# Kernel tuning notes

Hardware: AMD Instinct MI355X
Metric: run time of the kernel (lower is better)

Reference implementation:

```python
import jax, jax.numpy as jnp
import numpy as np

B, S, H, NH, FF = 8, 512, 1024, 16, 4096
DK = H // NH


def _ln(x, g, b):
    m = x.mean(-1, keepdims=True)
    v = ((x - m) ** 2).mean(-1, keepdims=True)
    return (x - m) / jnp.sqrt(v + 1e-5) * g + b


def _fwd(x, predicate_pos, attn_bias, attention_mask, atom_graph, variable_graph,
         ln1_g, ln1_b, wq, bq, wk, bk, wv, bv, wo, bo,
         pq_w, pq_b, pk_w, pk_b, pv_w, pv_b, ln2_g, ln2_b, w1, b1, w2, b2):
    b_, s_, h_ = x.shape
    y = _ln(x, ln1_g, ln1_b)
    # ---- self attention (manual MHA with additive bias + mask) ----
    scale = DK ** -0.5
    q = (y @ wq + bq).reshape(b_, s_, NH, DK) * scale
    k = (y @ wk + bk).reshape(b_, s_, NH, DK)
    v = (y @ wv + bv).reshape(b_, s_, NH, DK)
    scores = jnp.einsum('bihd,bjhd->bhij', q, k)
    scores = scores + attn_bias[:, None, :, :] + attention_mask[:, None, :, :]
    att = jax.nn.softmax(scores, axis=-1)
    y_self = jnp.einsum('bhij,bjhd->bihd', att, v).reshape(b_, s_, h_) @ wo + bo
    # ---- path attention (single-head with graph biases) ----
    pscale = h_ ** -0.5
    pq = (y @ pq_w + pq_b) * pscale
    pk = y @ pk_w + pk_b
    pv = y @ pv_w + pv_b
    patt = jnp.einsum('bid,bjd->bij', pq, pk) + atom_graph + variable_graph
    patt = jax.nn.softmax(patt, axis=-1)
    xp = jnp.einsum('bij,bjd->bid', patt, pv)  # [B,S,H]
    # vectorized gather-mean over predicate positions (replaces per-sample loop)
    prev = jnp.concatenate([xp[:, :1], xp[:, :-1]], axis=1)   # xp[i-1]
    nxt = jnp.concatenate([xp[:, 1:], xp[:, -1:]], axis=1)    # xp[i+1]
    a0 = xp[:, 0:2].mean(axis=1, keepdims=True)               # i == 0
    a1 = xp[:, 0:3].mean(axis=1, keepdims=True)               # i == 1
    a2 = (xp + nxt) / 2.0                                     # pos[i-2] == 1
    a3 = (prev + xp + nxt) / 3.0                              # else
    i_arr = jnp.arange(s_)
    pos = (predicate_pos == 1)
    pos_m2 = jnp.pad(pos[:, :-2], ((0, 0), (2, 0)))           # pos[i-2], False for i<2
    atom = jnp.where(pos_m2[..., None], a2, a3)
    atom = jnp.where((i_arr == 1)[None, :, None], a1, atom)
    atom = jnp.where((i_arr == 0)[None, :, None], a0, atom)
    w = pos.astype(xp.dtype)
    path = (atom * w[..., None]).sum(1) / w.sum(1, keepdims=True)  # [B,H]
    y_path = jnp.broadcast_to(path[:, None, :], (b_, s_, h_))
    # ---- combine + residual + FFN ----
    x = x + (y_self + y_path) / 2.0
    y2 = _ln(x, ln2_g, ln2_b)
    hmid = jax.nn.gelu(y2 @ w1 + b1, approximate=False)
    return x + (hmid @ w2 + b2)


def setup_inputs() -> dict:
    key = jax.random.key(0)
    ks = jax.random.split(key, 16)
    def w(k, shape):
        return 0.02 * jax.random.normal(k, shape, dtype=jnp.float32)
    pp = jax.random.randint(ks[0], (B, S), 0, 2, dtype=jnp.int32)
    pp = pp.at[:, 2].set(1).at[:, -1].set(0)  # >=1 predicate; no predicate at last node
    return {
        'x': jax.random.normal(ks[1], (B, S, H), dtype=jnp.float32),
        'predicate_pos': pp,
        'variable_tags': jnp.zeros((B, S), dtype=jnp.int32),
        'attn_bias': 0.1 * jax.random.normal(ks[2], (B, S, S), dtype=jnp.float32),
        'attention_mask': jnp.zeros((B, S, S), dtype=jnp.float32),
        'atom_graph': 0.1 * jax.random.normal(ks[3], (B, S, S), dtype=jnp.float32),
        'variable_graph': 0.1 * jax.random.normal(ks[4], (B, S, S), dtype=jnp.float32),
        'ln1_g': jnp.ones((H,), jnp.float32), 'ln1_b': jnp.zeros((H,), jnp.float32),
        'wq': w(ks[5], (H, H)), 'bq': jnp.zeros((H,), jnp.float32),
        'wk': w(ks[6], (H, H)), 'bk': jnp.zeros((H,), jnp.float32),
        'wv': w(ks[7], (H, H)), 'bv': jnp.zeros((H,), jnp.float32),
        'wo': w(ks[8], (H, H)), 'bo': jnp.zeros((H,), jnp.float32),
        'pq_w': w(ks[9], (H, H)), 'pq_b': jnp.zeros((H,), jnp.float32),
        'pk_w': w(ks[10], (H, H)), 'pk_b': jnp.zeros((H,), jnp.float32),
        'pv_w': w(ks[11], (H, H)), 'pv_b': jnp.zeros((H,), jnp.float32),
        'ln2_g': jnp.ones((H,), jnp.float32), 'ln2_b': jnp.zeros((H,), jnp.float32),
        'w1': w(ks[12], (H, FF)), 'b1': jnp.zeros((FF,), jnp.float32),
        'w2': w(ks[13], (FF, H)), 'b2': jnp.zeros((H,), jnp.float32),
    }


def reference(x, predicate_pos, variable_tags, attn_bias, attention_mask, atom_graph, variable_graph,
              ln1_g, ln1_b, wq, bq, wk, bk, wv, bv, wo, bo,
              pq_w, pq_b, pk_w, pk_b, pv_w, pv_b, ln2_g, ln2_b, w1, b1, w2, b2):
    # variable_tags is unused in the original forward as well
    return _fwd(x, predicate_pos, attn_bias, attention_mask, atom_graph, variable_graph,
                ln1_g, ln1_b, wq, bq, wk, bk, wv, bv, wo, bo,
                pq_w, pq_b, pk_w, pk_b, pv_w, pv_b, ln2_g, ln2_b, w1, b1, w2, b2)
```

## Files before the change

### kernel.cpp

```cpp
#include <hip/hip_runtime.h>
#include <hip/hip_bf16.h>
#include <math.h>


typedef __bf16 bf16x8 __attribute__((ext_vector_type(8)));
typedef float f32x4 __attribute__((ext_vector_type(4)));

__device__ __forceinline__ void async_copy16(void* lds, const void* g) {
  __builtin_amdgcn_global_load_lds(
      (__attribute__((address_space(1))) void*)(void*)g,
      (__attribute__((address_space(3))) void*)lds, 16, 0, 0);
}

__global__ __launch_bounds__(256) void ln_rows_bf16(
    const float* __restrict__ X, const float* __restrict__ G,
    const float* __restrict__ Bt, __hip_bfloat16* __restrict__ O) {
  long row = blockIdx.x;
  int t = threadIdx.x;
  const float4 xv = ((const float4*)(X + row * 1024))[t];
  float s = xv.x + xv.y + xv.z + xv.w;
  float q = xv.x * xv.x + xv.y * xv.y + xv.z * xv.z + xv.w * xv.w;
#pragma unroll
  for (int o = 32; o; o >>= 1) {
    s += __shfl_xor(s, o);
    q += __shfl_xor(q, o);
  }
  __shared__ float rs[4], rq[4];
  int wid = t >> 6;
  if ((t & 63) == 0) { rs[wid] = s; rq[wid] = q; }
  __syncthreads();
  s = rs[0] + rs[1] + rs[2] + rs[3];
  q = rq[0] + rq[1] + rq[2] + rq[3];
  float mean = s * (1.f / 1024.f);
  float var = q * (1.f / 1024.f) - mean * mean;
  float rstd = rsqrtf(var + 1e-5f);
  const float4 gv = ((const float4*)G)[t];
  const float4 bv = ((const float4*)Bt)[t];
  __hip_bfloat16* o = O + row * 1024 + t * 4;
  o[0] = __float2bfloat16((xv.x - mean) * rstd * gv.x + bv.x);
  o[1] = __float2bfloat16((xv.y - mean) * rstd * gv.y + bv.y);
  o[2] = __float2bfloat16((xv.z - mean) * rstd * gv.z + bv.z);
  o[3] = __float2bfloat16((xv.w - mean) * rstd * gv.w + bv.w);
}

struct TC7 {
  const float* in[7];
  __hip_bfloat16* out[7];
  float scale[7];
};
__global__ __launch_bounds__(256) void tconv7(TC7 p) {
  __shared__ float t[32][33];
  int j = blockIdx.z;
  const float* in = p.in[j];
  __hip_bfloat16* out = p.out[j];
  float sc = p.scale[j];
  int c0 = blockIdx.x * 32, r0 = blockIdx.y * 32;
  int tid = threadIdx.x;
  int lr = tid >> 3, lc = (tid & 7) * 4;
  const float4 v = *(const float4*)&in[(long)(r0 + lr) * 1024 + c0 + lc];
  t[lr][lc] = v.x; t[lr][lc + 1] = v.y; t[lr][lc + 2] = v.z; t[lr][lc + 3] = v.w;
  __syncthreads();
  int oc = tid >> 3, orr = (tid & 7) * 4;
  __hip_bfloat16* o = &out[(long)(c0 + oc) * 1024 + r0 + orr];
  o[0] = __float2bfloat16(t[orr][oc] * sc);
  o[1] = __float2bfloat16(t[orr + 1][oc] * sc);
  o[2] = __float2bfloat16(t[orr + 2][oc] * sc);
  o[3] = __float2bfloat16(t[orr + 3][oc] * sc);
}

__global__ __launch_bounds__(256) void tconv_f32_bf16(
    const float* __restrict__ in, __hip_bfloat16* __restrict__ out, int R,
    int C) {
  __shared__ float t[32][33];
  int c0 = blockIdx.x * 32, r0 = blockIdx.y * 32;
  int tid = threadIdx.x;
  int lr = tid >> 3, lc = (tid & 7) * 4;
  const float4 v = *(const float4*)&in[(long)(r0 + lr) * C + c0 + lc];
  t[lr][lc] = v.x; t[lr][lc + 1] = v.y; t[lr][lc + 2] = v.z; t[lr][lc + 3] = v.w;
  __syncthreads();
  int oc = tid >> 3, orr = (tid & 7) * 4;
  __hip_bfloat16* o = &out[(long)(c0 + oc) * R + r0 + orr];
  o[0] = __float2bfloat16(t[orr][oc]);
  o[1] = __float2bfloat16(t[orr + 1][oc]);
  o[2] = __float2bfloat16(t[orr + 2][oc]);
  o[3] = __float2bfloat16(t[orr + 3][oc]);
}

__global__ __launch_bounds__(256) void tconv_bf16(
    const __hip_bfloat16* __restrict__ in, __hip_bfloat16* __restrict__ out,
    int R, int C, int ldin, long sIn) {
  __shared__ __hip_bfloat16 t[32][34];
  int bz = blockIdx.z;
  long ibase = (long)bz * sIn;
  long obase = (long)bz * R * C;
  int c0 = blockIdx.x * 32, r0 = blockIdx.y * 32;
  int tid = threadIdx.x;
  int lr = tid >> 3, lc = (tid & 7) * 4;
  const __hip_bfloat16* ip = &in[ibase + (long)(r0 + lr) * ldin + c0 + lc];
  t[lr][lc] = ip[0]; t[lr][lc + 1] = ip[1]; t[lr][lc + 2] = ip[2]; t[lr][lc + 3] = ip[3];
  __syncthreads();
  int oc = tid >> 3, orr = (tid & 7) * 4;
  __hip_bfloat16* o = &out[obase + (long)(c0 + oc) * R + r0 + orr];
  o[0] = t[orr][oc];
  o[1] = t[orr + 1][oc];
  o[2] = t[orr + 2][oc];
  o[3] = t[orr + 3][oc];
}

struct BC6 {
  const float* b[6];
  float scale[6];
};
__global__ __launch_bounds__(256) void bias_concat(BC6 p, float* __restrict__ o) {
  int idx = blockIdx.x * 256 + threadIdx.x;
  int j = idx >> 10, e = idx & 1023;
  o[idx] = p.b[j][e] * p.scale[j];
}

template <int BN>
__global__ __launch_bounds__(512, 2) void gemm256(
    const __hip_bfloat16* __restrict__ A, const __hip_bfloat16* __restrict__ Bt,
    const float* __restrict__ bias, void* __restrict__ C, int K, int lda,
    int ldb, int ldc, int act, int obf, long sC) {
  constexpr int NR = BN / 64;
  constexpr int ABYTES = 256 * 128;
  constexpr int BBYTES = BN * 128;
  constexpr int BUF = ABYTES + BBYTES;
  __shared__ char lds[2 * BUF];

  int nwg = gridDim.x * gridDim.y;
  int wg = blockIdx.y * gridDim.x + blockIdx.x;
  int cpx = nwg >> 3;
  int sw = (wg & 7) * cpx + (wg >> 3);
  int bx = sw % gridDim.x, by = sw / gridDim.x;
  const int m0 = by * 256, n0 = bx * BN;
  const int z = blockIdx.z;
  const long kbase = (long)z * K * 2;

  const int tid = threadIdx.x;
  const int lane = tid & 63, wid = tid >> 6;
  const int wm = wid >> 2, wn = wid & 3;
  const int ll = lane & 15, lh = lane >> 4;

  const char* Ag = (const char*)A;
  const char* Bg = (const char*)Bt;
  const int srow = tid >> 3;
  const int scb = (tid & 7) * 16;

  auto stage = [&](int t, int bsel) {
    char* base = lds + bsel * BUF;
    long kb = kbase + (long)t * 128;
#pragma unroll
    for (int l = 0; l < 4; ++l) {
      int row = l * 64 + srow;
      async_copy16(base + row * 128 + scb,
                   Ag + ((long)(m0 + row) * lda) * 2 + kb + scb);
    }
#pragma unroll
    for (int l = 0; l < BN / 64; ++l) {
      int row = l * 64 + srow;
      async_copy16(base + ABYTES + row * 128 + scb,
                   Bg + ((long)(n0 + row) * ldb) * 2 + kb + scb);
    }
  };

  f32x4 acc[8][NR];
#pragma unroll
  for (int m = 0; m < 8; ++m)
#pragma unroll
    for (int n = 0; n < NR; ++n) acc[m][n] = (f32x4){0.f, 0.f, 0.f, 0.f};

  const int nt = K >> 6;
  stage(0, 0);
  asm volatile("s_waitcnt vmcnt(0)" ::: "memory");
  __builtin_amdgcn_s_barrier();

  for (int t = 0; t < nt; ++t) {
    int bt = t & 1;
    if (t + 1 < nt) stage(t + 1, bt ^ 1);
    const char* Ab = lds + bt * BUF;
    const char* Bb = Ab + ABYTES;
#pragma unroll
    for (int ks = 0; ks < 2; ++ks) {
      bf16x8 af[8], bf[NR];
#pragma unroll
      for (int m = 0; m < 8; ++m)
        af[m] = *(const bf16x8*)(Ab + (wm * 128 + m * 16 + ll) * 128 +
                                 ks * 64 + lh * 16);
#pragma unroll
      for (int n = 0; n < NR; ++n)
        bf[n] = *(const bf16x8*)(Bb + (wn * (BN / 4) + n * 16 + ll) * 128 +
                                 ks * 64 + lh * 16);
      __builtin_amdgcn_s_setprio(1);
#pragma unroll
      for (int m = 0; m < 8; ++m)
#pragma unroll
        for (int n = 0; n < NR; ++n)
          acc[m][n] = __builtin_amdgcn_mfma_f32_16x16x32_bf16(af[m], bf[n],
                                                              acc[m][n], 0, 0, 0);
      __builtin_amdgcn_s_setprio(0);
    }
    asm volatile("s_waitcnt vmcnt(0)" ::: "memory");
    __builtin_amdgcn_s_barrier();
  }

#pragma unroll
  for (int m = 0; m < 8; ++m) {
    int row = m0 + wm * 128 + m * 16 + lh * 4;
#pragma unroll
    for (int n = 0; n < NR; ++n) {
      int col = n0 + wn * (BN / 4) + n * 16 + ll;
      float bs = bias ? bias[col] : 0.f;
#pragma unroll
      for (int r = 0; r < 4; ++r) {
        float v = acc[m][n][r] + bs;
        if (act) v = v * 0.5f * (1.f + erff(v * 0.70710678118f));
        long cidx = (long)z * sC + (long)(row + r) * ldc + col;
        if (obf)
          ((__hip_bfloat16*)C)[cidx] = __float2bfloat16(v);
        else
          ((float*)C)[cidx] = v;
      }
    }
  }
}

__global__ __launch_bounds__(256) void ffn2_reduce(
    const float* __restrict__ P, const float* __restrict__ X2,
    const float* __restrict__ b2, float* __restrict__ OUT) {
  int i = blockIdx.x * 256 + threadIdx.x;
  const long SP = 4194304;
  float4 a = ((const float4*)P)[i];
  float4 b = ((const float4*)(P + SP))[i];
  float4 c = ((const float4*)(P + 2 * SP))[i];
  float4 d = ((const float4*)(P + 3 * SP))[i];
  float4 xr = ((const float4*)X2)[i];
  const float4 bb = *(const float4*)(b2 + ((i & 255) * 4));
  float4 o;
  o.x = a.x + b.x + c.x + d.x + xr.x + bb.x;
  o.y = a.y + b.y + c.y + d.y + xr.y + bb.y;
  o.z = a.z + b.z + c.z + d.z + xr.z + bb.z;
  o.w = a.w + b.w + c.w + d.w + xr.w + bb.w;
  ((float4*)OUT)[i] = o;
}

__global__ __launch_bounds__(256) void gemm_bf16_nt(
    const __hip_bfloat16* __restrict__ A, const __hip_bfloat16* __restrict__ Bt,
    const float* __restrict__ bias, const float* __restrict__ E1,
    const float* __restrict__ E2, void* __restrict__ C, int K, int lda,
    int ldb, int ldc, long sA, long sB, long sC, long sE, float alpha, int act,
    int obf) {
  __shared__ unsigned short AsU[128 * 32];
  __shared__ unsigned short BsU[128 * 32];
  const int tid = threadIdx.x;
  const int lane = tid & 63, wave = tid >> 6;
  const int wr = wave >> 1, wc = wave & 1;

  int nwg = gridDim.x * gridDim.y;
  int wg = blockIdx.y * gridDim.x + blockIdx.x;
  int bx = blockIdx.x, by = blockIdx.y;
  if ((nwg & 7) == 0) {
    int cpx = nwg >> 3;
    int sw = (wg & 7) * cpx + (wg >> 3);
    bx = sw % gridDim.x;
    by = sw / gridDim.x;
  }
  const int m0 = by * 128, n0 = bx * 128;
  const int bz = blockIdx.z;
  const char* Ab = (const char*)(A + (long)bz * sA);
  const char* Bb = (const char*)(Bt + (long)bz * sB);

  f32x4 acc[4][4];
#pragma unroll
  for (int m = 0; m < 4; ++m)
#pragma unroll
    for (int n = 0; n < 4; ++n) acc[m][n] = (f32x4){0.f, 0.f, 0.f, 0.f};

  const int srow = tid >> 2;
  const int scol = (tid & 3) * 16;
  const int wbase = (tid >> 6) * 1024;

  for (int k0 = 0; k0 < K; k0 += 32) {
#pragma unroll
    for (int i = 0; i < 2; ++i) {
      async_copy16((char*)AsU + i * 4096 + wbase,
                   Ab + ((long)(m0 + i * 64 + srow) * lda + k0) * 2 + scol);
      async_copy16((char*)BsU + i * 4096 + wbase,
                   Bb + ((long)(n0 + i * 64 + srow) * ldb + k0) * 2 + scol);
    }
    __syncthreads();

    const int koff = (lane >> 4) * 8;
    bf16x8 a[4], b[4];
#pragma unroll
    for (int m = 0; m < 4; ++m)
      a[m] = *(const bf16x8*)&AsU[(wr * 64 + m * 16 + (lane & 15)) * 32 + koff];
#pragma unroll
    for (int n = 0; n < 4; ++n)
      b[n] = *(const bf16x8*)&BsU[(wc * 64 + n * 16 + (lane & 15)) * 32 + koff];
#pragma unroll
    for (int m = 0; m < 4; ++m)
#pragma unroll
      for (int n = 0; n < 4; ++n)
        acc[m][n] = __builtin_amdgcn_mfma_f32_16x16x32_bf16(a[m], b[n],
                                                            acc[m][n], 0, 0, 0);
    __syncthreads();
  }

#pragma unroll
  for (int m = 0; m < 4; ++m) {
    int row = m0 + wr * 64 + m * 16 + (lane >> 4) * 4;
#pragma unroll
    for (int n = 0; n < 4; ++n) {
      int col = n0 + wc * 64 + n * 16 + (lane & 15);
      float bs = bias ? bias[col] : 0.f;
#pragma unroll
      for (int r = 0; r < 4; ++r) {
        float v = (acc[m][n][r] + bs) * alpha;
        long eidx = (long)bz * sE + (long)(row + r) * ldc + col;
        if (E1) v += E1[eidx];
        if (E2) v += E2[eidx];
        if (act) v = v * 0.5f * (1.f + erff(v * 0.70710678118f));
        long cidx = (long)bz * sC + (long)(row + r) * ldc + col;
        if (obf)
          ((__hip_bfloat16*)C)[cidx] = __float2bfloat16(v);
        else
          ((float*)C)[cidx] = v;
      }
    }
  }
}

__global__ __launch_bounds__(256) void attn_mfma(
    const __hip_bfloat16* __restrict__ Q, const __hip_bfloat16* __restrict__ K,
    const __hip_bfloat16* __restrict__ VT, const float* __restrict__ BiasP,
    const float* __restrict__ MaskP, __hip_bfloat16* __restrict__ O,
    int ldqk) {
  __shared__ __hip_bfloat16 P[32][520];
  __shared__ float red[2][32][4];
  const int it = blockIdx.x, h = blockIdx.y, b = blockIdx.z;
  const int i0 = it * 32;
  const int tid = threadIdx.x;
  const int lane = tid & 63, w = tid >> 6;
  const int lh = lane >> 4, ll = lane & 15;

  const long qkb = (long)b * 512 * ldqk + h * 64;

  bf16x8 a[2][2];
#pragma unroll
  for (int m = 0; m < 2; ++m)
#pragma unroll
    for (int ks = 0; ks < 2; ++ks)
      a[m][ks] = *(const bf16x8*)&Q[qkb + (long)(i0 + m * 16 + ll) * ldqk +
                                    ks * 32 + lh * 8];

  f32x4 acc[2][8];
#pragma unroll
  for (int m = 0; m < 2; ++m)
#pragma unroll
    for (int n = 0; n < 8; ++n) acc[m][n] = (f32x4){0.f, 0.f, 0.f, 0.f};

#pragma unroll
  for (int n = 0; n < 8; ++n) {
    const __hip_bfloat16* kp =
        &K[qkb + (long)(w * 128 + n * 16 + ll) * ldqk + lh * 8];
    bf16x8 b0 = *(const bf16x8*)&kp[0];
    bf16x8 b1 = *(const bf16x8*)&kp[32];
#pragma unroll
    for (int m = 0; m < 2; ++m) {
      acc[m][n] =
          __builtin_amdgcn_mfma_f32_16x16x32_bf16(a[m][0], b0, acc[m][n], 0, 0, 0);
      acc[m][n] =
          __builtin_amdgcn_mfma_f32_16x16x32_bf16(a[m][1], b1, acc[m][n], 0, 0, 0);
    }
  }

  const long bmo = ((long)b * 512 + i0) * 512 + w * 128;
#pragma unroll
  for (int m = 0; m < 2; ++m)
#pragma unroll
    for (int r = 0; r < 4; ++r) {
      int row = m * 16 + lh * 4 + r;
#pragma unroll
      for (int n = 0; n < 8; ++n) {
        long gi = bmo + (long)row * 512 + n * 16 + ll;
        acc[m][n][r] += BiasP[gi] + MaskP[gi];
      }
    }

  float rmax[2][4];
#pragma unroll
  for (int m = 0; m < 2; ++m)
#pragma unroll
    for (int r = 0; r < 4; ++r) {
      float v = acc[m][0][r];
#pragma unroll
      for (int n = 1; n < 8; ++n) v = fmaxf(v, acc[m][n][r]);
#pragma unroll
      for (int o = 1; o < 16; o <<= 1) v = fmaxf(v, __shfl_xor(v, o));
      rmax[m][r] = v;
    }
  if (ll == 0) {
#pragma unroll
    for (int m = 0; m < 2; ++m)
#pragma unroll
      for (int r = 0; r < 4; ++r) red[0][m * 16 + lh * 4 + r][w] = rmax[m][r];
  }
  __syncthreads();
#pragma unroll
  for (int m = 0; m < 2; ++m)
#pragma unroll
    for (int r = 0; r < 4; ++r) {
      const float* p = red[0][m * 16 + lh * 4 + r];
      rmax[m][r] = fmaxf(fmaxf(p[0], p[1]), fmaxf(p[2], p[3]));
    }
  float rsum[2][4];
#pragma unroll
  for (int m = 0; m < 2; ++m)
#pragma unroll
    for (int r = 0; r < 4; ++r) {
      float s = 0.f;
#pragma unroll
      for (int n = 0; n < 8; ++n) {
        float e = __expf(acc[m][n][r] - rmax[m][r]);
        acc[m][n][r] = e;
        s += e;
      }
#pragma unroll
      for (int o = 1; o < 16; o <<= 1) s += __shfl_xor(s, o);
      rsum[m][r] = s;
    }
  if (ll == 0) {
#pragma unroll
    for (int m = 0; m < 2; ++m)
#pragma unroll
      for (int r = 0; r < 4; ++r) red[1][m * 16 + lh * 4 + r][w] = rsum[m][r];
  }
  __syncthreads();
#pragma unroll
  for (int m = 0; m < 2; ++m)
#pragma unroll
    for (int r = 0; r < 4; ++r) {
      const float* p = red[1][m * 16 + lh * 4 + r];
      float inv = 1.f / (p[0] + p[1] + p[2] + p[3]);
      int row = m * 16 + lh * 4 + r;
#pragma unroll
      for (int n = 0; n < 8; ++n)
        P[row][w * 128 + n * 16 + ll] = __float2bfloat16(acc[m][n][r] * inv);
    }
  __syncthreads();

  const long vtb = ((long)b * 1024 + h * 64) * 512;
  const long ob = (long)b * 512 * 1024 + h * 64;
  const int mw = (w >> 1) * 16, nw = (w & 1) * 32;
  f32x4 oacc[2];
  oacc[0] = (f32x4){0.f, 0.f, 0.f, 0.f};
  oacc[1] = (f32x4){0.f, 0.f, 0.f, 0.f};
#pragma unroll
  for (int ks = 0; ks < 16; ++ks) {
    int k0 = ks * 32;
    bf16x8 pa = *(const bf16x8*)&P[mw + ll][k0 + lh * 8];
#pragma unroll
    for (int nf = 0; nf < 2; ++nf) {
      bf16x8 vb = *(const bf16x8*)&VT[vtb + (long)(nw + nf * 16 + ll) * 512 +
                                      k0 + lh * 8];
      oacc[nf] =
          __builtin_amdgcn_mfma_f32_16x16x32_bf16(pa, vb, oacc[nf], 0, 0, 0);
    }
  }
#pragma unroll
  for (int nf = 0; nf < 2; ++nf)
#pragma unroll
    for (int r = 0; r < 4; ++r)
      O[ob + (long)(i0 + mw + lh * 4 + r) * 1024 + nw + nf * 16 + ll] =
          __float2bfloat16(oacc[nf][r]);
}

__global__ __launch_bounds__(256) void softmax_rows(
    const float* __restrict__ P, __hip_bfloat16* __restrict__ Ob) {
  const float* row = P + (long)blockIdx.x * 512;
  __hip_bfloat16* orow = Ob + (long)blockIdx.x * 512;
  int t = threadIdx.x;
  float v0 = row[t], v1 = row[t + 256];
  float m = fmaxf(v0, v1);
#pragma unroll
  for (int o = 32; o; o >>= 1) m = fmaxf(m, __shfl_xor(m, o));
  __shared__ float red[8];
  int wid = t >> 6, lane = t & 63;
  if (!lane) red[wid] = m;
  __syncthreads();
  m = fmaxf(fmaxf(red[0], red[1]), fmaxf(red[2], red[3]));
  float e0 = __expf(v0 - m), e1 = __expf(v1 - m);
  float s = e0 + e1;
#pragma unroll
  for (int o = 32; o; o >>= 1) s += __shfl_xor(s, o);
  if (!lane) red[4 + wid] = s;
  __syncthreads();
  s = red[4] + red[5] + red[6] + red[7];
  float inv = 1.f / s;
  orow[t] = __float2bfloat16(e0 * inv);
  orow[t + 256] = __float2bfloat16(e1 * inv);
}

__global__ __launch_bounds__(256) void path_partial(
    const float* __restrict__ xp, const int* __restrict__ pp,
    float* __restrict__ PP, float* __restrict__ WS) {
  int b = blockIdx.x, hc = blockIdx.y, ic = blockIdx.z;
  int h = hc * 256 + threadIdx.x;
  const int* ppb = pp + b * 512;
  const float* xb = xp + (long)b * 512 * 1024;
  int iA = ic * 64, iB = iA + 64;
  float acc = 0.f;
  for (int i = iA; i < iB; ++i) {
    if (ppb[i] != 1) continue;
    float cur = xb[(long)i * 1024 + h];
    float a;
    if (i == 0) {
      a = 0.5f * (cur + xb[1024 + h]);
    } else if (i == 1) {
      a = (xb[h] + cur + xb[2 * 1024 + h]) * (1.f / 3.f);
    } else {
      int inx = (i + 1 < 512) ? i + 1 : 511;
      float nx = xb[(long)inx * 1024 + h];
      if (ppb[i - 2] == 1) {
        a = 0.5f * (cur + nx);
      } else {
        a = (xb[(long)(i - 1) * 1024 + h] + cur + nx) * (1.f / 3.f);
      }
    }
    acc += a;
  }
  PP[((long)b * 8 + ic) * 1024 + h] = acc;
  if (hc == 0 && threadIdx.x == 0) {
    float c = 0.f;
    for (int i = iA; i < iB; ++i) c += (ppb[i] == 1) ? 1.f : 0.f;
    WS[b * 8 + ic] = c;
  }
}

__global__ __launch_bounds__(256) void path_finalize(
    const float* __restrict__ PP, const float* __restrict__ WS,
    float* __restrict__ PATH) {
  int b = blockIdx.x;
  int h = blockIdx.y * 256 + threadIdx.x;
  float s = 0.f, w = 0.f;
#pragma unroll
  for (int ic = 0; ic < 8; ++ic) {
    s += PP[((long)b * 8 + ic) * 1024 + h];
    w += WS[b * 8 + ic];
  }
  PATH[b * 1024 + h] = s / w;
}

__global__ __launch_bounds__(256) void combine_ln2(
    const float* __restrict__ X, const float* __restrict__ YS,
    const float* __restrict__ PT, const float* __restrict__ G,
    const float* __restrict__ Bt, float* __restrict__ X2,
    __hip_bfloat16* __restrict__ Y2b) {
  long row = blockIdx.x;
  int b = (int)(row >> 9);
  int t = threadIdx.x;
  const float4 xv = ((const float4*)(X + row * 1024))[t];
  const float4 sv = ((const float4*)(YS + row * 1024))[t];
  const float4 pv = *(const float4*)(PT + b * 1024 + t * 4);
  float4 v;
  v.x = xv.x + 0.5f * (sv.x + pv.x);
  v.y = xv.y + 0.5f * (sv.y + pv.y);
  v.z = xv.z + 0.5f * (sv.z + pv.z);
  v.w = xv.w + 0.5f * (sv.w + pv.w);
  ((float4*)(X2 + row * 1024))[t] = v;

  float s = v.x + v.y + v.z + v.w;
  float q = v.x * v.x + v.y * v.y + v.z * v.z + v.w * v.w;
#pragma unroll
  for (int o = 32; o; o >>= 1) {
    s += __shfl_xor(s, o);
    q += __shfl_xor(q, o);
  }
  __shared__ float rs[4], rq[4];
  int wid = t >> 6;
  if ((t & 63) == 0) { rs[wid] = s; rq[wid] = q; }
  __syncthreads();
  s = rs[0] + rs[1] + rs[2] + rs[3];
  q = rq[0] + rq[1] + rq[2] + rq[3];
  float mean = s * (1.f / 1024.f);
  float var = q * (1.f / 1024.f) - mean * mean;
  float rstd = rsqrtf(var + 1e-5f);
  const float4 gv = ((const float4*)G)[t];
  const float4 bv = ((const float4*)Bt)[t];
  __hip_bfloat16* o = Y2b + row * 1024 + t * 4;
  o[0] = __float2bfloat16((v.x - mean) * rstd * gv.x + bv.x);
  o[1] = __float2bfloat16((v.y - mean) * rstd * gv.y + bv.y);
  o[2] = __float2bfloat16((v.z - mean) * rstd * gv.z + bv.z);
  o[3] = __float2bfloat16((v.w - mean) * rstd * gv.w + bv.w);
}

extern "C" void kernel_launch(void* const* d_in, const int* in_sizes, int n_in,
                              void* d_out, int out_size, void* d_ws,
                              size_t ws_size, hipStream_t stream) {
  const float* x = (const float*)d_in[0];
  const int* pp = (const int*)d_in[1];
  const float* abias = (const float*)d_in[3];
  const float* amask = (const float*)d_in[4];
  const float* agraph = (const float*)d_in[5];
  const float* vgraph = (const float*)d_in[6];
  const float* ln1g = (const float*)d_in[7];
  const float* ln1b = (const float*)d_in[8];
  const float* wq = (const float*)d_in[9];
  const float* bq = (const float*)d_in[10];
  const float* wk = (const float*)d_in[11];
  const float* bk = (const float*)d_in[12];
  const float* wv = (const float*)d_in[13];
  const float* bv = (const float*)d_in[14];
  const float* wo = (const float*)d_in[15];
  const float* bo = (const float*)d_in[16];
  const float* pqw = (const float*)d_in[17];
  const float* pqb = (const float*)d_in[18];
  const float* pkw = (const float*)d_in[19];
  const float* pkb = (const float*)d_in[20];
  const float* pvw = (const float*)d_in[21];
  const float* pvb = (const float*)d_in[22];
  const float* ln2g = (const float*)d_in[23];
  const float* ln2b = (const float*)d_in[24];
  const float* w1 = (const float*)d_in[25];
  const float* b1 = (const float*)d_in[26];
  const float* w2 = (const float*)d_in[27];
  const float* b2 = (const float*)d_in[28];

  char* wsb = (char*)d_ws;
  auto Ybf = (__hip_bfloat16*)(wsb);
  auto QKV = (__hip_bfloat16*)(wsb + (8l << 20));
  auto VTb = (__hip_bfloat16*)(wsb + (56l << 20));
  auto PVT = (__hip_bfloat16*)(wsb + (64l << 20));
  auto ATTb = (__hip_bfloat16*)(wsb + (72l << 20));
  auto PATTb = (__hip_bfloat16*)(wsb + (88l << 20));
  auto PATTf = (float*)(wsb + (92l << 20));
  auto XP = (float*)(wsb + (92l << 20));
  auto WALL = (__hip_bfloat16*)(wsb + (108l << 20));
  auto WOT = (__hip_bfloat16*)(wsb + (120l << 20));
  auto W1T = (__hip_bfloat16*)(wsb + (122l << 20));
  auto bias6 = (float*)(wsb + (130l << 20));
  auto PPart = (float*)(wsb + (131l << 20));
  auto WSp = (float*)(wsb + (132l << 20));
  auto PATH = (float*)(wsb + (133l << 20));
  auto YSELF = (float*)(wsb + (8l << 20));
  auto X2 = (float*)(wsb + (24l << 20));
  auto HMID = (__hip_bfloat16*)(wsb + (40l << 20));
  auto W2T = ATTb;
  auto PART = (float*)(wsb + (92l << 20));
  __hip_bfloat16* Y2b = Ybf;
  float* OUT = (float*)d_out;

  const float qscale = 0.125f;
  const float pscale = 0.03125f;
  const long S2 = 512l * 512;
  const long SQ = 512l * 6144;

  __hip_bfloat16* Qp = QKV;
  __hip_bfloat16* Kp = QKV + 1024;
  __hip_bfloat16* Vp = QKV + 2048;
  __hip_bfloat16* PQp = QKV + 3072;
  __hip_bfloat16* PKp = QKV + 4096;
  __hip_bfloat16* PVp = QKV + 5120;

  TC7 tp;
  tp.in[0] = wq;  tp.out[0] = WALL;                 tp.scale[0] = qscale;
  tp.in[1] = wk;  tp.out[1] = WALL + 1024 * 1024;   tp.scale[1] = 1.f;
  tp.in[2] = wv;  tp.out[2] = WALL + 2048 * 1024;   tp.scale[2] = 1.f;
  tp.in[3] = pqw; tp.out[3] = WALL + 3072 * 1024;   tp.scale[3] = pscale;
  tp.in[4] = pkw; tp.out[4] = WALL + 4096 * 1024;   tp.scale[4] = 1.f;
  tp.in[5] = pvw; tp.out[5] = WALL + 5120 * 1024;   tp.scale[5] = 1.f;
  tp.in[6] = wo;  tp.out[6] = WOT;                  tp.scale[6] = 1.f;
  tconv7<<<dim3(32, 32, 7), 256, 0, stream>>>(tp);
  tconv_f32_bf16<<<dim3(128, 32), 256, 0, stream>>>(w1, W1T, 1024, 4096);

  BC6 bp;
  bp.b[0] = bq;  bp.scale[0] = qscale;
  bp.b[1] = bk;  bp.scale[1] = 1.f;
  bp.b[2] = bv;  bp.scale[2] = 1.f;
  bp.b[3] = pqb; bp.scale[3] = pscale;
  bp.b[4] = pkb; bp.scale[4] = 1.f;
  bp.b[5] = pvb; bp.scale[5] = 1.f;
  bias_concat<<<24, 256, 0, stream>>>(bp, bias6);

  ln_rows_bf16<<<4096, 256, 0, stream>>>(x, ln1g, ln1b, Ybf);

  gemm256<128><<<dim3(48, 16, 1), 512, 0, stream>>>(
      Ybf, WALL, bias6, QKV, 1024, 1024, 1024, 6144, 0, 1, 0);

  tconv_bf16<<<dim3(32, 16, 8), 256, 0, stream>>>(Vp, VTb, 512, 1024, 6144, SQ);
  tconv_bf16<<<dim3(32, 16, 8), 256, 0, stream>>>(PVp, PVT, 512, 1024, 6144, SQ);

  gemm_bf16_nt<<<dim3(4, 4, 8), 256, 0, stream>>>(
      PQp, PKp, nullptr, agraph, vgraph, PATTf, 1024, 6144, 6144, 512, SQ, SQ,
      S2, S2, 1.f, 0, 0);
  softmax_rows<<<4096, 256, 0, stream>>>(PATTf, PATTb);

  attn_mfma<<<dim3(16, 16, 8), 256, 0, stream>>>(Qp, Kp, VTb, abias, amask,
                                                 ATTb, 6144);

  gemm_bf16_nt<<<dim3(8, 4, 8), 256, 0, stream>>>(
      PATTb, PVT, nullptr, nullptr, nullptr, XP, 512, 512, 512, 1024, S2,
      512l * 1024, 512l * 1024, 0, 1.f, 0, 0);

  path_partial<<<dim3(8, 4, 8), 256, 0, stream>>>(XP, pp, PPart, WSp);
  path_finalize<<<dim3(8, 4), 256, 0, stream>>>(PPart, WSp, PATH);

  gemm_bf16_nt<<<dim3(8, 32, 1), 256, 0, stream>>>(
      ATTb, WOT, bo, nullptr, nullptr, YSELF, 1024, 1024, 1024, 1024, 0, 0, 0,
      0, 1.f, 0, 0);

  tconv_f32_bf16<<<dim3(32, 128), 256, 0, stream>>>(w2, W2T, 4096, 1024);

  combine_ln2<<<4096, 256, 0, stream>>>(x, YSELF, PATH, ln2g, ln2b, X2, Y2b);

  gemm256<256><<<dim3(16, 16, 1), 512, 0, stream>>>(
      Y2b, W1T, b1, HMID, 1024, 1024, 1024, 4096, 1, 1, 0);

  gemm256<128><<<dim3(8, 16, 4), 512, 0, stream>>>(
      HMID, W2T, nullptr, PART, 1024, 4096, 4096, 1024, 0, 0, 4194304);

  ffn2_reduce<<<4096, 256, 0, stream>>>(PART, X2, b2, OUT);
}
```

Baseline: 530.1 us.

## Swizzle GEMM LDS layout, remap XCD tiles, and overlap next-stage loads

The GEMM kernel now applies an XOR swizzle to the K-chunk position of each row, so LDS fragment reads avoid bank conflicts. Workgroups are remapped so each XCD gets a contiguous 2D block of output tiles, which should improve L2 reuse. The full vmcnt(0) wait at the end of each iteration is replaced with a partial wait after issuing the next stage, so prefetch loads stay in flight during the MFMA work. This relies on exact vmcnt counts matching the number of copies per stage, and a mismatch would cause races.

```diff
diff --git a/kernel.cpp b/kernel.cpp
--- a/kernel.cpp
+++ b/kernel.cpp
@@ -128,11 +128,20 @@
   constexpr int BUF = ABYTES + BBYTES;
   __shared__ char lds[2 * BUF];
 
-  int nwg = gridDim.x * gridDim.y;
-  int wg = blockIdx.y * gridDim.x + blockIdx.x;
-  int cpx = nwg >> 3;
-  int sw = (wg & 7) * cpx + (wg >> 3);
-  int bx = sw % gridDim.x, by = sw / gridDim.x;
+  int bx, by;
+  {
+    int wg = blockIdx.y * gridDim.x + blockIdx.x;
+    int gx = gridDim.x, gy = gridDim.y;
+    if ((gx & 3) == 0 && (gy & 1) == 0) {
+      int cw = gx >> 2, ch = gy >> 1;
+      int xcd = wg & 7, idx = wg >> 3;
+      bx = (xcd & 3) * cw + idx % cw;
+      by = (xcd >> 2) * ch + idx / cw;
+    } else {
+      bx = blockIdx.x;
+      by = blockIdx.y;
+    }
+  }
   const int m0 = by * 256, n0 = bx * BN;
   const int z = blockIdx.z;
   const long kbase = (long)z * K * 2;
@@ -145,7 +154,8 @@
   const char* Ag = (const char*)A;
   const char* Bg = (const char*)Bt;
   const int srow = tid >> 3;
-  const int scb = (tid & 7) * 16;
+  const int scb = (((tid & 7) ^ (srow & 7)) << 4);
+  const int sld = (tid & 7) << 4;
 
   auto stage = [&](int t, int bsel) {
     char* base = lds + bsel * BUF;
@@ -153,16 +163,19 @@
 #pragma unroll
     for (int l = 0; l < 4; ++l) {
       int row = l * 64 + srow;
-      async_copy16(base + row * 128 + scb,
+      async_copy16(base + row * 128 + sld,
                    Ag + ((long)(m0 + row) * lda) * 2 + kb + scb);
     }
 #pragma unroll
     for (int l = 0; l < BN / 64; ++l) {
       int row = l * 64 + srow;
-      async_copy16(base + ABYTES + row * 128 + scb,
+      async_copy16(base + ABYTES + row * 128 + sld,
                    Bg + ((long)(n0 + row) * ldb) * 2 + kb + scb);
     }
   };
+
+  const int rx = ll & 7;
+  const int ck[2] = {((0 + lh) ^ rx) << 4, ((4 + lh) ^ rx) << 4};
 
   f32x4 acc[8][NR];
 #pragma unroll
@@ -172,12 +185,21 @@
 
   const int nt = K >> 6;
   stage(0, 0);
-  asm volatile("s_waitcnt vmcnt(0)" ::: "memory");
-  __builtin_amdgcn_s_barrier();
 
   for (int t = 0; t < nt; ++t) {
     int bt = t & 1;
-    if (t + 1 < nt) stage(t + 1, bt ^ 1);
+    if (t + 1 < nt) {
+      stage(t + 1, bt ^ 1);
+      if constexpr (BN == 128)
+        asm volatile("s_waitcnt vmcnt(6)" ::: "memory");
+      else
+        asm volatile("s_waitcnt vmcnt(8)" ::: "memory");
+    } else {
+      asm volatile("s_waitcnt vmcnt(0)" ::: "memory");
+    }
+    __builtin_amdgcn_s_barrier();
+    __builtin_amdgcn_sched_barrier(0);
+
     const char* Ab = lds + bt * BUF;
     const char* Bb = Ab + ABYTES;
 #pragma unroll
@@ -185,12 +207,11 @@
       bf16x8 af[8], bf[NR];
 #pragma unroll
       for (int m = 0; m < 8; ++m)
-        af[m] = *(const bf16x8*)(Ab + (wm * 128 + m * 16 + ll) * 128 +
-                                 ks * 64 + lh * 16);
+        af[m] = *(const bf16x8*)(Ab + (wm * 128 + m * 16 + ll) * 128 + ck[ks]);
 #pragma unroll
       for (int n = 0; n < NR; ++n)
         bf[n] = *(const bf16x8*)(Bb + (wn * (BN / 4) + n * 16 + ll) * 128 +
-                                 ks * 64 + lh * 16);
+                                 ck[ks]);
       __builtin_amdgcn_s_setprio(1);
 #pragma unroll
       for (int m = 0; m < 8; ++m)
@@ -200,7 +221,7 @@
                                                               acc[m][n], 0, 0, 0);
       __builtin_amdgcn_s_setprio(0);
     }
-    asm volatile("s_waitcnt vmcnt(0)" ::: "memory");
+    __builtin_amdgcn_sched_barrier(0);
     __builtin_amdgcn_s_barrier();
   }
 
```

Result: faster. 481.7 us (-9.1%).
